# Kernel optimization log

Hardware: AMD Instinct MI355X
Metric: run time of the kernel (lower is better)

Reference implementation:

```python
import jax, jax.numpy as jnp
import numpy as np

SCALE = 128.0  # init arg; divisor is sqrt(scale)
NEG_BIG = -1e10

def setup_inputs() -> dict:
    key = jax.random.key(0)
    kq, kk, kv, km = jax.random.split(key, 4)
    B, Nq, Nk, D = 16, 2048, 2048, 128
    q = jax.random.normal(kq, (B, Nq, D), dtype=jnp.float32)
    k = jax.random.normal(kk, (B, Nk, D), dtype=jnp.float32)
    v = jax.random.normal(kv, (B, Nk, D), dtype=jnp.float32)
    mask = jax.random.randint(km, (B, Nq, Nk), 0, 2).astype(bool)
    return {"q": q, "k": k, "v": v, "mask": mask}

def reference(q, k, v, mask):
    inv = 1.0 / np.sqrt(SCALE).astype(np.float32)
    # scores: [b, q, k]
    scores = jnp.einsum('bqd,bkd->bqk', q, k) * inv
    scores = jnp.where(mask, NEG_BIG, scores)
    att = jax.nn.softmax(scores, axis=-1)
    context = jnp.einsum('bqk,bkd->bqd', att, v)
    return (context, att)
```

## Files before the change

### kernel.cpp

```cpp
#include <hip/hip_runtime.h>

#define B_ 16
#define NQ 2048
#define NK 2048
#define DH 128
#define INV 0.08838834764831843f
#define QSCALE (0.08838834764831843f * 1.4426950408889634f)

typedef __attribute__((ext_vector_type(8))) short bf16x8;
typedef __attribute__((ext_vector_type(4))) float f32x4;

typedef const __attribute__((address_space(1))) unsigned int* gas1_t;
typedef __attribute__((address_space(3))) unsigned int* las3_t;

#define VMW(n)   asm volatile("s_waitcnt vmcnt(" #n ")" ::: "memory")
#define BARRIER() do { __builtin_amdgcn_s_barrier(); asm volatile("" ::: "memory"); } while (0)

__device__ __forceinline__ unsigned short f2b(float f) {
  unsigned u = __float_as_uint(f);
  u += 0x7fff + ((u >> 16) & 1);
  return (unsigned short)(u >> 16);
}

__device__ __forceinline__ void gl_lds16(const unsigned short* g, unsigned short* l) {
  __builtin_amdgcn_global_load_lds((gas1_t)g, (las3_t)l, 16, 0, 0);
}

__global__ __launch_bounds__(256) void k_cvt(
    const float* __restrict__ src, unsigned short* __restrict__ dst, int n4,
    float scale) {
  int i = blockIdx.x * 256 + threadIdx.x;
  if (i >= n4) return;
  float4 f = ((const float4*)src)[i];
  ushort4 u;
  u.x = f2b(f.x * scale); u.y = f2b(f.y * scale);
  u.z = f2b(f.z * scale); u.w = f2b(f.w * scale);
  ((ushort4*)dst)[i] = u;
}

__global__ __launch_bounds__(256) void k_trans(
    const float* __restrict__ v, unsigned short* __restrict__ vt) {
  __shared__ float tile[32][33];
  const int b = blockIdx.z, kv0 = blockIdx.x << 5, d0 = blockIdx.y << 5;
  const int tx = threadIdx.x & 31, ty = threadIdx.x >> 5;
  #pragma unroll
  for (int i = 0; i < 4; i++)
    tile[ty + 8*i][tx] = v[((size_t)b*NK + kv0 + ty + 8*i)*DH + d0 + tx];
  __syncthreads();
  #pragma unroll
  for (int i = 0; i < 4; i++)
    vt[((size_t)b*DH + d0 + ty + 8*i)*NK + kv0 + tx] = f2b(tile[tx][ty + 8*i]);
}

__global__ __launch_bounds__(256, 4) void k_attn(
    const unsigned short* __restrict__ qb, const unsigned short* __restrict__ kb,
    const unsigned short* __restrict__ vtb, const int* __restrict__ mask,
    float* __restrict__ att, float* __restrict__ ctx) {
  __shared__ unsigned short KA[64*128];
  __shared__ unsigned short VA[128*64];
  __shared__ unsigned short Ps[32*64];
  __shared__ float Lrow[32];

  const int t = threadIdx.x;
  const int wave = t >> 6, lane = t & 63, quad = lane >> 4, l15 = lane & 15;
  const int rh = wave >> 1, nh = wave & 1;

  const int p = blockIdx.x + (blockIdx.y << 6);
  const int lid = ((p & 7) << 7) + (p >> 3);
  const int b = lid >> 6, q0 = (lid & 63) << 5;

  const unsigned short* qg = qb  + ((size_t)b*NQ + q0)*DH;
  const unsigned short* kg = kb  + (size_t)b*NK*DH;
  const unsigned short* vg = vtb + (size_t)b*DH*NK;
  const int* mg   = mask + ((size_t)b*NQ + q0)*NK;
  float*     attg = att  + ((size_t)b*NQ + q0)*NK;
  float*     cg   = ctx  + ((size_t)b*NQ + q0)*DH;

  if (t < 32) Lrow[t] = 0.f;

  bf16x8 qf[4];
  { const unsigned short* qr = qg + (size_t)(rh*16 + l15)*DH + quad*8;
    #pragma unroll
    for (int kd = 0; kd < 4; kd++) qf[kd] = *(const bf16x8*)(qr + kd*32); }

  const int row0 = rh*16 + quad*4;
  const int* mgR[4]; float* attR[4];
  #pragma unroll
  for (int r = 0; r < 4; r++) {
    mgR[r]  = mg   + (size_t)(row0 + r)*NK + nh*32 + l15;
    attR[r] = attg + (size_t)(row0 + r)*NK + nh*32 + l15;
  }

  const int kr0 = nh*32 + l15, kr1 = kr0 + 16;
  const int kbs0 = (kr0 << 8) ^ ((kr0 & 7) << 4);
  const int kbs1 = (kr1 << 8) ^ ((kr1 & 7) << 4);
  const int pr  = rh*16 + l15;
  const int pbs = (pr << 7) ^ ((pr & 7) << 4);
  int vbs[4];
  #pragma unroll
  for (int dt = 0; dt < 4; dt++) {
    int d = nh*64 + dt*16 + l15;
    vbs[dt] = (d << 7) ^ ((d & 7) << 4);
  }

  auto stageK = [&](unsigned short* buf, const unsigned short* src) {
    #pragma unroll
    for (int i = 0; i < 4; i++) {
      int L = (wave << 12) + (i << 10) + (lane << 4);
      int row = L >> 8;
      int cb  = (L & 255) ^ ((row & 7) << 4);
      gl_lds16(src + ((size_t)row << 7) + (cb >> 1), buf + (L >> 1));
    }
  };
  auto stageV = [&](const unsigned short* src) {
    #pragma unroll
    for (int i = 0; i < 4; i++) {
      int L = (wave << 12) + (i << 10) + (lane << 4);
      int d  = L >> 7;
      int cb = (L & 127) ^ ((d & 7) << 4);
      gl_lds16(src + (size_t)d*NK + (cb >> 1), VA + (L >> 1));
    }
  };
  auto loadMask = [&](int k0, int* mr) {
    #pragma unroll
    for (int nt = 0; nt < 2; nt++)
      #pragma unroll
      for (int r = 0; r < 4; r++)
        mr[nt*4 + r] = __builtin_nontemporal_load(mgR[r] + k0 + nt*16);
  };
  auto qkt = [&](const unsigned short* buf, f32x4& s0v, f32x4& s1v) {
    s0v = 0; s1v = 0;
    const char* bc = (const char*)buf;
    __builtin_amdgcn_s_setprio(1);
    #pragma unroll
    for (int kd = 0; kd < 4; kd++) {
      int cb = (kd*32 + quad*8) << 1;
      bf16x8 b0 = *(const bf16x8*)(bc + (kbs0 ^ cb));
      bf16x8 b1 = *(const bf16x8*)(bc + (kbs1 ^ cb));
      s0v = __builtin_amdgcn_mfma_f32_16x16x32_bf16(qf[kd], b0, s0v, 0, 0, 0);
      s1v = __builtin_amdgcn_mfma_f32_16x16x32_bf16(qf[kd], b1, s1v, 0, 0, 0);
    }
    __builtin_amdgcn_s_setprio(0);
  };

  float ls[4] = {0.f, 0.f, 0.f, 0.f};

  auto epi1 = [&](const int* mr, const f32x4& s0v, const f32x4& s1v) -> unsigned {
    unsigned nb = 0;
    #pragma unroll
    for (int nt = 0; nt < 2; nt++) {
      const f32x4& sv = nt ? s1v : s0v;
      #pragma unroll
      for (int r = 0; r < 4; r++) {
        float e = __builtin_amdgcn_exp2f(sv[r]);
        if (mr[nt*4 + r] != 0) { nb |= 1u << (nt*4 + r); e = 0.f; }
        ls[r] += e;
      }
    }
    return nb;
  };

  unsigned mw0=0,mw1=0,mw2=0,mw3=0,mw4=0,mw5=0,mw6=0,mw7=0;

  int mrA[8], mrB[8], mrC[8], mrD[8];
  stageK(KA, kg);                 loadMask(0,    mrA);
  stageK(VA, kg + (size_t)64*DH); loadMask(64,   mrB);

#define S1_STEP(RDBUF, MR, SH, VN) do {                                  \
    VMW(VN); BARRIER();                                                  \
    f32x4 s0, s1; qkt(RDBUF, s0, s1);                                    \
    bw |= epi1(MR, s0, s1) << SH;                                        \
    BARRIER(); } while (0)

  for (int t2 = 0; t2 < 28; t2 += 4) {
    unsigned bw = 0;
    S1_STEP(KA, mrA, 0, 12);
    stageK(KA, kg + (size_t)(t2+2)*64*DH); loadMask((t2+2)*64, mrC);
    S1_STEP(VA, mrB, 8, 12);
    stageK(VA, kg + (size_t)(t2+3)*64*DH); loadMask((t2+3)*64, mrD);
    S1_STEP(KA, mrC, 16, 12);
    stageK(KA, kg + (size_t)(t2+4)*64*DH); loadMask((t2+4)*64, mrA);
    S1_STEP(VA, mrD, 24, 12);
    stageK(VA, kg + (size_t)(t2+5)*64*DH); loadMask((t2+5)*64, mrB);
    mw0=mw1; mw1=mw2; mw2=mw3; mw3=mw4; mw4=mw5; mw5=mw6; mw6=mw7; mw7=bw;
  }
  {
    unsigned bw = 0;
    S1_STEP(KA, mrA, 0, 12);
    stageK(KA, kg + (size_t)30*64*DH); loadMask(30*64, mrC);
    S1_STEP(VA, mrB, 8, 12);
    stageK(VA, kg + (size_t)31*64*DH); loadMask(31*64, mrD);
    S1_STEP(KA, mrC, 16, 12);
    S1_STEP(VA, mrD, 24, 0);
    mw0=mw1; mw1=mw2; mw2=mw3; mw3=mw4; mw4=mw5; mw5=mw6; mw6=mw7; mw7=bw;
  }
#undef S1_STEP

  __syncthreads();
  #pragma unroll
  for (int r = 0; r < 4; r++) {
    float v = ls[r];
    v += __shfl_xor(v, 1); v += __shfl_xor(v, 2);
    v += __shfl_xor(v, 4); v += __shfl_xor(v, 8);
    if (l15 == 0) atomicAdd(&Lrow[row0 + r], v);
  }
  __syncthreads();
  float il[4];
  #pragma unroll
  for (int r = 0; r < 4; r++) il[r] = 1.0f / Lrow[row0 + r];

  f32x4 ca[4];
  #pragma unroll
  for (int dt = 0; dt < 4; dt++) ca[dt] = 0;

  stageK(KA, kg);
  for (int t4 = 0; t4 < 32; t4 += 4) {
    unsigned cw = mw0;
    mw0=mw1; mw1=mw2; mw2=mw3; mw3=mw4; mw4=mw5; mw5=mw6; mw6=mw7;
    #pragma unroll
    for (int k = 0; k < 4; k++) {
      const int tt = t4 + k;
      BARRIER();
      stageV(vg + tt*64);
      VMW(4);
      BARRIER();
      f32x4 s0, s1;
      qkt(KA, s0, s1);

      const unsigned nb = (cw >> (8*k)) & 255u;
      #pragma unroll
      for (int nt = 0; nt < 2; nt++) {
        const f32x4& sv = nt ? s1 : s0;
        #pragma unroll
        for (int r = 0; r < 4; r++) {
          float e = __builtin_amdgcn_exp2f(sv[r]) * il[r];
          if ((nb >> (nt*4 + r)) & 1) e = 0.f;
          attR[r][tt*64 + nt*16] = e;
          int row = row0 + r;
          int cbw = ((nh*32 + nt*16 + l15) << 1) ^ ((row & 7) << 4);
          *(unsigned short*)((char*)Ps + (row << 7) + cbw) = f2b(e);
        }
      }
      asm volatile("s_waitcnt vmcnt(8) lgkmcnt(0)" ::: "memory");
      BARRIER();
      if (tt + 1 < 32) stageK(KA, kg + (size_t)(tt+1)*64*DH);

      __builtin_amdgcn_s_setprio(1);
      #pragma unroll
      for (int kv = 0; kv < 2; kv++) {
        int cb = (kv*32 + quad*8) << 1;
        bf16x8 pa = *(const bf16x8*)((const char*)Ps + (pbs ^ cb));
        #pragma unroll
        for (int dt = 0; dt < 4; dt++) {
          bf16x8 vb = *(const bf16x8*)((const char*)VA + (vbs[dt] ^ cb));
          ca[dt] = __builtin_amdgcn_mfma_f32_16x16x32_bf16(pa, vb, ca[dt], 0, 0, 0);
        }
      }
      __builtin_amdgcn_s_setprio(0);
    }
  }

  #pragma unroll
  for (int dt = 0; dt < 4; dt++)
    #pragma unroll
    for (int r = 0; r < 4; r++)
      cg[(size_t)(row0 + r)*DH + nh*64 + dt*16 + l15] = ca[dt][r];
}

extern "C" void kernel_launch(void* const* d_in, const int* in_sizes, int n_in,
                              void* d_out, int out_size, void* d_ws, size_t ws_size,
                              hipStream_t stream) {
  const float* q = (const float*)d_in[0];
  const float* k = (const float*)d_in[1];
  const float* v = (const float*)d_in[2];
  const int* mask = (const int*)d_in[3];
  float* ctx = (float*)d_out;
  float* att = ctx + (size_t)B_*NQ*DH;

  const size_t NE = (size_t)B_*NQ*DH;
  unsigned short* qws = (unsigned short*)d_ws;
  unsigned short* kws = qws + NE;
  unsigned short* vws = kws + NE;

  k_cvt  <<<(int)(NE/1024), 256, 0, stream>>>(q, qws, (int)(NE/4), QSCALE);
  k_cvt  <<<(int)(NE/1024), 256, 0, stream>>>(k, kws, (int)(NE/4), 1.0f);
  k_trans<<<dim3(NK/32, DH/32, B_), 256, 0, stream>>>(v, vws);
  k_attn <<<dim3(NQ/32, B_), 256, 0, stream>>>(qws, kws, vws, mask, att, ctx);
}
```

Before: 582.0 us.

## Double-buffer K tiles with dedicated KB buffer in both attention passes

Adds a second K tile buffer (KB) so pass 1 ping-pongs K between KA and KB with a one-tile prefetch, no longer borrowing VA as a K buffer and dropping the trailing barrier per step. In pass 2, the next K tile is prefetched into the alternate buffer together with the V tile, so the K load overlaps the PV MFMA instead of being issued after the softmax writes. This adds 16KB of LDS per block, which may reduce occupancy under the launch bounds of 4 blocks, and it changes the vmcnt wait thresholds, which have to match the number of outstanding loads exactly.

```diff
diff --git a/kernel.cpp b/kernel.cpp
--- a/kernel.cpp
+++ b/kernel.cpp
@@ -4,7 +4,6 @@
 #define NQ 2048
 #define NK 2048
 #define DH 128
-#define INV 0.08838834764831843f
 #define QSCALE (0.08838834764831843f * 1.4426950408889634f)
 
 typedef __attribute__((ext_vector_type(8))) short bf16x8;
@@ -57,6 +56,7 @@
     const unsigned short* __restrict__ vtb, const int* __restrict__ mask,
     float* __restrict__ att, float* __restrict__ ctx) {
   __shared__ unsigned short KA[64*128];
+  __shared__ unsigned short KB[64*128];
   __shared__ unsigned short VA[128*64];
   __shared__ unsigned short Ps[32*64];
   __shared__ float Lrow[32];
@@ -162,39 +162,38 @@
 
   unsigned mw0=0,mw1=0,mw2=0,mw3=0,mw4=0,mw5=0,mw6=0,mw7=0;
 
-  int mrA[8], mrB[8], mrC[8], mrD[8];
-  stageK(KA, kg);                 loadMask(0,    mrA);
-  stageK(VA, kg + (size_t)64*DH); loadMask(64,   mrB);
-
-#define S1_STEP(RDBUF, MR, SH, VN) do {                                  \
+  int mrA[8], mrB[8];
+  stageK(KA, kg);
+  loadMask(0, mrA);
+
+#define S1_STEP(T, RD, WR, MRC, MRN, VN) do {                            \
+    BARRIER();                                                           \
+    if ((T) + 1 < 32) {                                                  \
+      stageK(WR, kg + (size_t)((T)+1)*64*DH);                            \
+      loadMask(((T)+1)*64, MRN);                                         \
+    }                                                                    \
     VMW(VN); BARRIER();                                                  \
-    f32x4 s0, s1; qkt(RDBUF, s0, s1);                                    \
-    bw |= epi1(MR, s0, s1) << SH;                                        \
-    BARRIER(); } while (0)
+    f32x4 s0, s1; qkt(RD, s0, s1);                                       \
+    bw |= epi1(MRC, s0, s1) << (8*((T)&3)); } while (0)
 
   for (int t2 = 0; t2 < 28; t2 += 4) {
     unsigned bw = 0;
-    S1_STEP(KA, mrA, 0, 12);
-    stageK(KA, kg + (size_t)(t2+2)*64*DH); loadMask((t2+2)*64, mrC);
-    S1_STEP(VA, mrB, 8, 12);
-    stageK(VA, kg + (size_t)(t2+3)*64*DH); loadMask((t2+3)*64, mrD);
-    S1_STEP(KA, mrC, 16, 12);
-    stageK(KA, kg + (size_t)(t2+4)*64*DH); loadMask((t2+4)*64, mrA);
-    S1_STEP(VA, mrD, 24, 12);
-    stageK(VA, kg + (size_t)(t2+5)*64*DH); loadMask((t2+5)*64, mrB);
+    S1_STEP(t2+0, KA, KB, mrA, mrB, 12);
+    S1_STEP(t2+1, KB, KA, mrB, mrA, 12);
+    S1_STEP(t2+2, KA, KB, mrA, mrB, 12);
+    S1_STEP(t2+3, KB, KA, mrB, mrA, 12);
     mw0=mw1; mw1=mw2; mw2=mw3; mw3=mw4; mw4=mw5; mw5=mw6; mw6=mw7; mw7=bw;
   }
-  {
-    unsigned bw = 0;
-    S1_STEP(KA, mrA, 0, 12);
-    stageK(KA, kg + (size_t)30*64*DH); loadMask(30*64, mrC);
-    S1_STEP(VA, mrB, 8, 12);
-    stageK(VA, kg + (size_t)31*64*DH); loadMask(31*64, mrD);
-    S1_STEP(KA, mrC, 16, 12);
-    S1_STEP(VA, mrD, 24, 0);
+  { unsigned bw = 0;
+    S1_STEP(28, KA, KB, mrA, mrB, 12);
+    S1_STEP(29, KB, KA, mrB, mrA, 12);
+    S1_STEP(30, KA, KB, mrA, mrB, 12);
+    S1_STEP(31, KB, KA, mrB, mrA, 0);
     mw0=mw1; mw1=mw2; mw2=mw3; mw3=mw4; mw4=mw5; mw5=mw6; mw6=mw7; mw7=bw;
   }
 #undef S1_STEP
+
+  stageK(KA, kg);
 
   __syncthreads();
   #pragma unroll
@@ -213,7 +212,8 @@
   #pragma unroll
   for (int dt = 0; dt < 4; dt++) ca[dt] = 0;
 
-  stageK(KA, kg);
+  VMW(0);
+
   for (int t4 = 0; t4 < 32; t4 += 4) {
     unsigned cw = mw0;
     mw0=mw1; mw1=mw2; mw2=mw3; mw3=mw4; mw4=mw5; mw5=mw6; mw6=mw7;
@@ -222,10 +222,12 @@
       const int tt = t4 + k;
       BARRIER();
       stageV(vg + tt*64);
-      VMW(4);
+      stageK((tt & 1) ? KA : KB,
+             kg + (size_t)((tt + 1) & 31)*64*DH);
+      VMW(16);
       BARRIER();
       f32x4 s0, s1;
-      qkt(KA, s0, s1);
+      qkt((tt & 1) ? KB : KA, s0, s1);
 
       const unsigned nb = (cw >> (8*k)) & 255u;
       #pragma unroll
@@ -241,10 +243,8 @@
           *(unsigned short*)((char*)Ps + (row << 7) + cbw) = f2b(e);
         }
       }
-      asm volatile("s_waitcnt vmcnt(8) lgkmcnt(0)" ::: "memory");
+      asm volatile("s_waitcnt vmcnt(12) lgkmcnt(0)" ::: "memory");
       BARRIER();
-      if (tt + 1 < 32) stageK(KA, kg + (size_t)(tt+1)*64*DH);
-
       __builtin_amdgcn_s_setprio(1);
       #pragma unroll
       for (int kv = 0; kv < 2; kv++) {
```

Measured after the change: 568.7 us. -2.3%, faster.
